# Optimization experiments

Hardware: AMD Instinct MI355X
Metric: run time of the kernel (lower is better)

The kernel has to match this reference:

```python
import jax, jax.numpy as jnp
import numpy as np

P = 512        # n_predicates
C = 65536      # n_constants
L = 1          # max_rule_length (only runnable config of original code)


def setup_inputs() -> dict:
    key = jax.random.key(0)
    k1, k2 = jax.random.split(key)
    initial_facts = jax.random.uniform(k1, (P, C), dtype=jnp.float32)
    rule_weights = jax.random.normal(k2, (P, L, P), dtype=jnp.float32)
    return {"initial_facts": initial_facts, "rule_weights": rule_weights, "n_iterations": 3}


def reference(initial_facts, rule_weights, n_iterations):
    # F.softmax(rule[step], dim=0) on the 1-D vector rule_weights[r, 0, :]
    # == softmax over the last axis of rule_weights[:, 0, :].
    # Stacking apply_rule over all rules r is exactly A @ facts.
    A = jax.nn.softmax(rule_weights[:, 0, :], axis=-1)  # [P, P]
    facts = initial_facts                                # [P, C]
    for _ in range(n_iterations):
        derived = A @ facts                              # [P, C] (rule r -> row r)
        facts = jnp.maximum(facts, derived.max(axis=0))  # broadcast [C] over [P, C]
    return facts
```

## Files before the change

### kernel.cpp

```cpp
#include <hip/hip_runtime.h>
#include <hip/hip_bf16.h>
#include <cstdint>


typedef __attribute__((ext_vector_type(8))) short bf16x8;
typedef __attribute__((ext_vector_type(4))) float f32x4;
typedef unsigned short ushort_t;
typedef unsigned int uint32;

#define PDIM 512
#define CDIM 65536
#define NT   64

__device__ __forceinline__ ushort_t f2bf(float x) {
    uint32 u = __float_as_uint(x);
    return (ushort_t)((u + 0x7fffu + ((u >> 16) & 1u)) >> 16);
}
__device__ __forceinline__ float bf2f(uint32 bits) { return __uint_as_float(bits << 16); }

__global__ __launch_bounds__(64) void softmax_pack(const float* __restrict__ rw,
                                                   ushort_t* __restrict__ Apk) {
    const int r  = blockIdx.x;
    const int ln = threadIdx.x;
    const float* row = rw + r * PDIM;
    float4 x0 = *(const float4*)(row + ln * 8);
    float4 x1 = *(const float4*)(row + ln * 8 + 4);
    float v[8] = {x0.x, x0.y, x0.z, x0.w, x1.x, x1.y, x1.z, x1.w};

    float mx = -1e30f;
    #pragma unroll
    for (int i = 0; i < 8; ++i) mx = fmaxf(mx, v[i]);
    #pragma unroll
    for (int d = 1; d < 64; d <<= 1) mx = fmaxf(mx, __shfl_xor(mx, d, 64));
    float s = 0.f;
    #pragma unroll
    for (int i = 0; i < 8; ++i) { v[i] = __expf(v[i] - mx); s += v[i]; }
    #pragma unroll
    for (int d = 1; d < 64; d <<= 1) s += __shfl_xor(s, d, 64);
    const float inv = 1.f / s;

    ushort_t o[8];
    #pragma unroll
    for (int i = 0; i < 8; ++i) o[i] = f2bf(v[i] * inv);
    const int idx16 = (ln >> 2) * 2048 + (r >> 4) * 64 + ((ln & 3) << 4) + (r & 15);
    *(int4*)(Apk + idx16 * 8) = *(const int4*)o;
}

__global__ __launch_bounds__(256, 2) void ilp_kernel(
        const float* __restrict__ facts,
        const ushort_t* __restrict__ Apk,
        int* __restrict__ gm,
        const int* __restrict__ n_iter_p,
        float* __restrict__ out) {
    __shared__ ushort_t ft[NT * PDIM];

    const int tid  = threadIdx.x;
    const int wave = tid >> 6;
    const int lane = tid & 63;
    const int l15  = lane & 15;
    const int quad = lane >> 4;
    const int c0   = blockIdx.x * NT;
    int* gmb = gm + blockIdx.x * NT;

    {
        if (tid < NT) gmb[tid] = (int)0x80000000;
        const int c  = tid & 63;
        const int pb = tid >> 6;
        for (int s = 0; s < 16; ++s) {
            const int p0 = s * 32 + pb * 8;
            ushort_t g[8];
            #pragma unroll
            for (int i = 0; i < 8; ++i)
                g[i] = f2bf(facts[(p0 + i) * CDIM + c0 + c]);
            const int gidx = (p0 >> 3) ^ (c & 7);
            *(int4*)(&ft[c * PDIM + gidx * 8]) = *(const int4*)g;
        }
    }
    __syncthreads();

    int n_iter = *n_iter_p;
    n_iter = n_iter < 0 ? 0 : (n_iter > 8 ? 8 : n_iter);

    const int abase = wave * 4096 + lane * 8;
    int cbase[4], cx8[4];
    #pragma unroll
    for (int ct = 0; ct < 4; ++ct) {
        const int c = ct * 16 + l15;
        cbase[ct] = c * PDIM;
        cx8[ct]   = (c & 7) * 8;
    }

    #pragma unroll 1
    for (int it = 0; it < n_iter; ++it) {
        f32x4 acc[8][4];
        #pragma unroll
        for (int rt = 0; rt < 8; ++rt)
            #pragma unroll
            for (int ct = 0; ct < 4; ++ct) acc[rt][ct] = (f32x4){0.f, 0.f, 0.f, 0.f};

        bf16x8 aF[2][8];
        {
            const ushort_t* ap = Apk + abase;
            #pragma unroll
            for (int rt = 0; rt < 8; ++rt) aF[0][rt] = *(const bf16x8*)(ap + rt * 512);
        }

        #pragma unroll 2
        for (int kt = 0; kt < 16; ++kt) {
            const int cur = kt & 1, nxt = cur ^ 1;
            bf16x8 bF[4];
            const int g8 = (kt * 4 + quad) * 8;
            #pragma unroll
            for (int ct = 0; ct < 4; ++ct)
                bF[ct] = *(const bf16x8*)(&ft[cbase[ct] + (g8 ^ cx8[ct])]);

            {
                const ushort_t* ap = Apk + abase + (((kt + 1) & 15) * 16384);
                #pragma unroll
                for (int rt = 0; rt < 8; ++rt) aF[nxt][rt] = *(const bf16x8*)(ap + rt * 512);
            }

            #pragma unroll
            for (int rt = 0; rt < 8; ++rt)
                #pragma unroll
                for (int ct = 0; ct < 4; ++ct)
                    acc[rt][ct] = __builtin_amdgcn_mfma_f32_16x16x32_bf16(
                        aF[cur][rt], bF[ct], acc[rt][ct], 0, 0, 0);
        }

        float mx[4] = {-1e30f, -1e30f, -1e30f, -1e30f};
        #pragma unroll
        for (int ct = 0; ct < 4; ++ct) {
            #pragma unroll
            for (int rt = 0; rt < 8; ++rt)
                #pragma unroll
                for (int e = 0; e < 4; ++e)
                    mx[ct] = fmaxf(mx[ct], acc[rt][ct][e]);
            mx[ct] = fmaxf(mx[ct], __shfl_xor(mx[ct], 16, 64));
            mx[ct] = fmaxf(mx[ct], __shfl_xor(mx[ct], 32, 64));
        }
        if (quad == 0) {
            #pragma unroll
            for (int ct = 0; ct < 4; ++ct)
                atomicMax(&gmb[ct * 16 + l15], __float_as_int(mx[ct]));
        }
        __syncthreads();

        if (it < n_iter - 1) {
            const int c = tid & 63;
            const int mbits = atomicMax(&gmb[c], (int)0x80000000);
            const uint32 ml = (uint32)f2bf(__int_as_float(mbits));
            #pragma unroll 1
            for (int j = 0; j < 16; ++j) {
                const int slot = (wave + 4 * j) ^ (c & 7);
                uint32* ptr = (uint32*)(&ft[c * PDIM + slot * 8]);
                uint4 v = *(uint4*)ptr;
                uint32* w = (uint32*)&v;
                #pragma unroll
                for (int q = 0; q < 4; ++q) {
                    uint32 lo = w[q] & 0xffffu, hi = w[q] >> 16;
                    lo = lo > ml ? lo : ml;
                    hi = hi > ml ? hi : ml;
                    w[q] = lo | (hi << 16);
                }
                *(uint4*)ptr = v;
            }
            __syncthreads();
        }
    }

    {
        const int c  = tid & 63;
        const int pb = tid >> 6;
        const int mbits = atomicMax(&gmb[c], (int)0x80000000);
        const float m = __int_as_float(mbits);
        for (int s = 0; s < 16; ++s) {
            const int p0 = s * 32 + pb * 8;
            const int gidx = (p0 >> 3) ^ (c & 7);
            ushort_t g[8];
            *(int4*)g = *(const int4*)(&ft[c * PDIM + gidx * 8]);
            #pragma unroll
            for (int i = 0; i < 8; ++i)
                out[(p0 + i) * CDIM + c0 + c] = fmaxf(bf2f(g[i]), m);
        }
    }
}

extern "C" void kernel_launch(void* const* d_in, const int* in_sizes, int n_in,
                              void* d_out, int out_size, void* d_ws, size_t ws_size,
                              hipStream_t stream) {
    const float* facts    = (const float*)d_in[0];
    const float* rw       = (const float*)d_in[1];
    const int*   n_iter_p = (const int*)d_in[2];
    float* out = (float*)d_out;

    ushort_t* Apk = (ushort_t*)d_ws;
    int*      gm  = (int*)((char*)d_ws + (size_t)PDIM * PDIM * 2);

    softmax_pack<<<PDIM, 64, 0, stream>>>(rw, Apk);
    ilp_kernel<<<CDIM / NT, 256, 0, stream>>>(facts, Apk, gm, n_iter_p, out);
}
```

Measured before the change: 331.1 us.

## Fold per-iteration max into B-fragment loads and reduce maxima via LDS

Drops the separate LDS pass that rewrote facts with the running column max between iterations. The max is now applied lazily as a packed bf16 max on each B fragment as it is loaded. Global atomics for the column max are replaced by a double-buffered LDS reduction across waves, and B fragments are double-buffered with MFMA priority raised. Global loads and stores are widened to float2. The change adds register pressure from the extra bF buffer and a VALU max on every B load.

```diff
diff --git a/kernel.cpp b/kernel.cpp
--- a/kernel.cpp
+++ b/kernel.cpp
@@ -4,6 +4,7 @@
 
 
 typedef __attribute__((ext_vector_type(8))) short bf16x8;
+typedef __attribute__((ext_vector_type(8))) unsigned short u16x8;
 typedef __attribute__((ext_vector_type(4))) float f32x4;
 typedef unsigned short ushort_t;
 typedef unsigned int uint32;
@@ -17,6 +18,13 @@
     return (ushort_t)((u + 0x7fffu + ((u >> 16) & 1u)) >> 16);
 }
 __device__ __forceinline__ float bf2f(uint32 bits) { return __uint_as_float(bits << 16); }
+
+__device__ __forceinline__ bf16x8 pkmax8(bf16x8 v, ushort_t mu) {
+    u16x8 a = __builtin_bit_cast(u16x8, v);
+    const u16x8 mb = {mu, mu, mu, mu, mu, mu, mu, mu};
+    a = __builtin_elementwise_max(a, mb);
+    return __builtin_bit_cast(bf16x8, a);
+}
 
 __global__ __launch_bounds__(64) void softmax_pack(const float* __restrict__ rw,
                                                    ushort_t* __restrict__ Apk) {
@@ -49,10 +57,11 @@
 __global__ __launch_bounds__(256, 2) void ilp_kernel(
         const float* __restrict__ facts,
         const ushort_t* __restrict__ Apk,
-        int* __restrict__ gm,
         const int* __restrict__ n_iter_p,
         float* __restrict__ out) {
     __shared__ ushort_t ft[NT * PDIM];
+    __shared__ float wred[2][4][NT];
+    __shared__ float mfin[NT];
 
     const int tid  = threadIdx.x;
     const int wave = tid >> 6;
@@ -60,20 +69,23 @@
     const int l15  = lane & 15;
     const int quad = lane >> 4;
     const int c0   = blockIdx.x * NT;
-    int* gmb = gm + blockIdx.x * NT;
 
     {
-        if (tid < NT) gmb[tid] = (int)0x80000000;
-        const int c  = tid & 63;
-        const int pb = tid >> 6;
-        for (int s = 0; s < 16; ++s) {
-            const int p0 = s * 32 + pb * 8;
-            ushort_t g[8];
-            #pragma unroll
-            for (int i = 0; i < 8; ++i)
-                g[i] = f2bf(facts[(p0 + i) * CDIM + c0 + c]);
-            const int gidx = (p0 >> 3) ^ (c & 7);
-            *(int4*)(&ft[c * PDIM + gidx * 8]) = *(const int4*)g;
+        const int ch = (tid & 31) * 2;
+        const int pb = tid >> 5;
+        #pragma unroll 4
+        for (int s = 0; s < 8; ++s) {
+            const int p0 = s * 64 + pb * 8;
+            ushort_t ga[8], gb[8];
+            #pragma unroll
+            for (int i = 0; i < 8; ++i) {
+                const float2 v = *(const float2*)(facts + (p0 + i) * CDIM + c0 + ch);
+                ga[i] = f2bf(v.x);
+                gb[i] = f2bf(v.y);
+            }
+            const int g = p0 >> 3;
+            *(int4*)(&ft[ch * PDIM + ((g ^ (ch & 7)) << 3)])             = *(const int4*)ga;
+            *(int4*)(&ft[(ch + 1) * PDIM + ((g ^ ((ch + 1) & 7)) << 3)]) = *(const int4*)gb;
         }
     }
     __syncthreads();
@@ -90,6 +102,16 @@
         cx8[ct]   = (c & 7) * 8;
     }
 
+    ushort_t ml[4] = {0, 0, 0, 0};
+    float    mf[4] = {0.f, 0.f, 0.f, 0.f};
+
+    bf16x8 aF[2][8], bF[2][4];
+    {
+        const ushort_t* ap = Apk + abase;
+        #pragma unroll
+        for (int rt = 0; rt < 8; ++rt) aF[0][rt] = *(const bf16x8*)(ap + rt * 512);
+    }
+
     #pragma unroll 1
     for (int it = 0; it < n_iter; ++it) {
         f32x4 acc[8][4];
@@ -98,90 +120,90 @@
             #pragma unroll
             for (int ct = 0; ct < 4; ++ct) acc[rt][ct] = (f32x4){0.f, 0.f, 0.f, 0.f};
 
-        bf16x8 aF[2][8];
         {
-            const ushort_t* ap = Apk + abase;
-            #pragma unroll
-            for (int rt = 0; rt < 8; ++rt) aF[0][rt] = *(const bf16x8*)(ap + rt * 512);
+            const int g8 = quad * 8;
+            #pragma unroll
+            for (int ct = 0; ct < 4; ++ct)
+                bF[0][ct] = pkmax8(*(const bf16x8*)(&ft[cbase[ct] + (g8 ^ cx8[ct])]), ml[ct]);
         }
 
         #pragma unroll 2
         for (int kt = 0; kt < 16; ++kt) {
             const int cur = kt & 1, nxt = cur ^ 1;
-            bf16x8 bF[4];
-            const int g8 = (kt * 4 + quad) * 8;
-            #pragma unroll
-            for (int ct = 0; ct < 4; ++ct)
-                bF[ct] = *(const bf16x8*)(&ft[cbase[ct] + (g8 ^ cx8[ct])]);
-
+            const int ktn = (kt + 1) & 15;
             {
-                const ushort_t* ap = Apk + abase + (((kt + 1) & 15) * 16384);
+                const ushort_t* ap = Apk + abase + ktn * 16384;
                 #pragma unroll
                 for (int rt = 0; rt < 8; ++rt) aF[nxt][rt] = *(const bf16x8*)(ap + rt * 512);
             }
-
+            {
+                const int g8 = (ktn * 4 + quad) * 8;
+                #pragma unroll
+                for (int ct = 0; ct < 4; ++ct)
+                    bF[nxt][ct] = pkmax8(*(const bf16x8*)(&ft[cbase[ct] + (g8 ^ cx8[ct])]), ml[ct]);
+            }
+            __builtin_amdgcn_s_setprio(1);
             #pragma unroll
             for (int rt = 0; rt < 8; ++rt)
                 #pragma unroll
                 for (int ct = 0; ct < 4; ++ct)
                     acc[rt][ct] = __builtin_amdgcn_mfma_f32_16x16x32_bf16(
-                        aF[cur][rt], bF[ct], acc[rt][ct], 0, 0, 0);
-        }
-
-        float mx[4] = {-1e30f, -1e30f, -1e30f, -1e30f};
+                        aF[cur][rt], bF[cur][ct], acc[rt][ct], 0, 0, 0);
+            __builtin_amdgcn_s_setprio(0);
+        }
+
+        float mx[4];
         #pragma unroll
         for (int ct = 0; ct < 4; ++ct) {
+            float m0 = -1e30f;
             #pragma unroll
             for (int rt = 0; rt < 8; ++rt)
                 #pragma unroll
-                for (int e = 0; e < 4; ++e)
-                    mx[ct] = fmaxf(mx[ct], acc[rt][ct][e]);
-            mx[ct] = fmaxf(mx[ct], __shfl_xor(mx[ct], 16, 64));
-            mx[ct] = fmaxf(mx[ct], __shfl_xor(mx[ct], 32, 64));
-        }
+                for (int e = 0; e < 4; ++e) m0 = fmaxf(m0, acc[rt][ct][e]);
+            m0 = fmaxf(m0, __shfl_xor(m0, 16, 64));
+            m0 = fmaxf(m0, __shfl_xor(m0, 32, 64));
+            mx[ct] = m0;
+        }
+        const int buf = it & 1;
         if (quad == 0) {
             #pragma unroll
-            for (int ct = 0; ct < 4; ++ct)
-                atomicMax(&gmb[ct * 16 + l15], __float_as_int(mx[ct]));
+            for (int ct = 0; ct < 4; ++ct) wred[buf][wave][ct * 16 + l15] = mx[ct];
         }
         __syncthreads();
-
-        if (it < n_iter - 1) {
-            const int c = tid & 63;
-            const int mbits = atomicMax(&gmb[c], (int)0x80000000);
-            const uint32 ml = (uint32)f2bf(__int_as_float(mbits));
-            #pragma unroll 1
-            for (int j = 0; j < 16; ++j) {
-                const int slot = (wave + 4 * j) ^ (c & 7);
-                uint32* ptr = (uint32*)(&ft[c * PDIM + slot * 8]);
-                uint4 v = *(uint4*)ptr;
-                uint32* w = (uint32*)&v;
-                #pragma unroll
-                for (int q = 0; q < 4; ++q) {
-                    uint32 lo = w[q] & 0xffffu, hi = w[q] >> 16;
-                    lo = lo > ml ? lo : ml;
-                    hi = hi > ml ? hi : ml;
-                    w[q] = lo | (hi << 16);
-                }
-                *(uint4*)ptr = v;
-            }
-            __syncthreads();
-        }
-    }
+        #pragma unroll
+        for (int ct = 0; ct < 4; ++ct) {
+            const int c = ct * 16 + l15;
+            const float m = fmaxf(fmaxf(wred[buf][0][c], wred[buf][1][c]),
+                                  fmaxf(wred[buf][2][c], wred[buf][3][c]));
+            mf[ct] = fmaxf(mf[ct], m);
+            ml[ct] = f2bf(mf[ct]);
+        }
+    }
+
+    if (wave == 0 && quad == 0) {
+        #pragma unroll
+        for (int ct = 0; ct < 4; ++ct) mfin[ct * 16 + l15] = mf[ct];
+    }
+    __syncthreads();
 
     {
-        const int c  = tid & 63;
-        const int pb = tid >> 6;
-        const int mbits = atomicMax(&gmb[c], (int)0x80000000);
-        const float m = __int_as_float(mbits);
-        for (int s = 0; s < 16; ++s) {
-            const int p0 = s * 32 + pb * 8;
-            const int gidx = (p0 >> 3) ^ (c & 7);
-            ushort_t g[8];
-            *(int4*)g = *(const int4*)(&ft[c * PDIM + gidx * 8]);
-            #pragma unroll
-            for (int i = 0; i < 8; ++i)
-                out[(p0 + i) * CDIM + c0 + c] = fmaxf(bf2f(g[i]), m);
+        const int ch = (tid & 31) * 2;
+        const int pb = tid >> 5;
+        const float ma = mfin[ch];
+        const float mb = mfin[ch + 1];
+        for (int s = 0; s < 8; ++s) {
+            const int p0 = s * 64 + pb * 8;
+            const int g = p0 >> 3;
+            ushort_t ga[8], gb[8];
+            *(int4*)ga = *(const int4*)(&ft[ch * PDIM + ((g ^ (ch & 7)) << 3)]);
+            *(int4*)gb = *(const int4*)(&ft[(ch + 1) * PDIM + ((g ^ ((ch + 1) & 7)) << 3)]);
+            #pragma unroll
+            for (int i = 0; i < 8; ++i) {
+                float2 v;
+                v.x = fmaxf(bf2f(ga[i]), ma);
+                v.y = fmaxf(bf2f(gb[i]), mb);
+                *(float2*)(out + (p0 + i) * CDIM + c0 + ch) = v;
+            }
         }
     }
 }
@@ -195,8 +217,7 @@
     float* out = (float*)d_out;
 
     ushort_t* Apk = (ushort_t*)d_ws;
-    int*      gm  = (int*)((char*)d_ws + (size_t)PDIM * PDIM * 2);
 
     softmax_pack<<<PDIM, 64, 0, stream>>>(rw, Apk);
-    ilp_kernel<<<CDIM / NT, 256, 0, stream>>>(facts, Apk, gm, n_iter_p, out);
-}
+    ilp_kernel<<<CDIM / NT, 256, 0, stream>>>(facts, Apk, n_iter_p, out);
+}
```

Measured after the change: 302.6 us. 8.6% less time.
